# Performance work log

Hardware: AMD Instinct MI355X
Metric: run time of the kernel (lower is better)

The kernel has to match this reference:

```python
import jax, jax.numpy as jnp
import numpy as np

BS, N, FIN = 128, 320, 1
H1, F1 = 8, 18   # layer-1 heads / hidden
H2, F2 = 4, 46   # layer-2 heads / hidden
D1 = H1 * F1     # 144
D2 = H2 * F2     # 184
FC = (104, 45, 84)
ALPHA = 0.2
NEG = -9e15


def _xavier(key, shape):
    fan_in, fan_out = shape[-2], shape[-1]
    s = 1.414 * np.sqrt(2.0 / (fan_in + fan_out))
    return jax.random.normal(key, shape, dtype=jnp.float32) * s


def setup_inputs() -> dict:
    key = jax.random.key(0)
    ks = jax.random.split(key, 20)
    xnodes = jax.random.normal(ks[0], (BS, N, FIN), dtype=jnp.float32)
    adj = (jax.random.uniform(ks[1], (N, N)) < 0.1).astype(jnp.float32)
    adj = jnp.maximum(adj, jnp.eye(N, dtype=jnp.float32))
    inp = {
        'xnodes': xnodes,
        'adj': adj,
        'W1': _xavier(ks[2], (H1, FIN, F1)),
        'a1': _xavier(ks[3], (H1, 2 * F1)),
        'W2': _xavier(ks[4], (H2, D1, F2)),
        'a2': _xavier(ks[5], (H2, 2 * F2)),
        'p1w': _xavier(ks[6], (D1, 1))[:, 0],
        'p1b': jnp.zeros((), jnp.float32),
        'p2w': _xavier(ks[7], (D2, 1))[:, 0],
        'p2b': jnp.zeros((), jnp.float32),
        'e1w': _xavier(ks[8], (3 * N, FC[0])),
        'e1b': jnp.zeros((FC[0],), jnp.float32),
        'e2w': _xavier(ks[9], (FC[0], FC[1])),
        'e2b': jnp.zeros((FC[1],), jnp.float32),
        'e3w': _xavier(ks[10], (FC[1], FC[2])),
        'e3b': jnp.zeros((FC[2],), jnp.float32),
        'cw': _xavier(ks[11], (FC[2], 1))[:, 0],
        'cb': jnp.zeros((), jnp.float32),
    }
    return inp


def _gat(x, adj_mask, W, a):
    """Multi-head GAT layer (all heads vectorized).
    x: [b,n,fin], W: [h,fin,f], a: [h,2f], adj_mask: [n,n] bool.
    Score e_ij = leakyrelu(a_src.h_i + a_dst.h_j) == concat-matmul of the
    original, without materializing the [b,n,n,2f] tensor.
    """
    h = jnp.einsum('bni,hif->bhnf', x, W)              # [b,h,n,f]
    f = h.shape[-1]
    es = jnp.einsum('bhnf,hf->bhn', h, a[:, :f])       # source term
    ed = jnp.einsum('bhnf,hf->bhn', h, a[:, f:])       # dest term
    e = jax.nn.leaky_relu(es[:, :, :, None] + ed[:, :, None, :], ALPHA)
    e = jnp.where(adj_mask[None, None], e, NEG)
    att = jax.nn.softmax(e, axis=-1)                   # [b,h,n,n]
    hp = jnp.einsum('bhnm,bhmf->bhnf', att, h)
    out = jax.nn.elu(hp)                               # concat=True
    b = out.shape[0]
    return out.transpose(0, 2, 1, 3).reshape(b, out.shape[2], -1)  # [b,n,h*f]


def reference(xnodes, adj, W1, a1, W2, a2, p1w, p1b, p2w, p2b,
              e1w, e1b, e2w, e2b, e3w, e3b, cw, cb):
    mask = adj > 0
    x0 = jnp.mean(xnodes, axis=-1)                     # [b,n]
    x = _gat(xnodes, mask, W1, a1)                     # [b,n,144]
    x1 = x @ p1w + p1b                                 # pool1 -> [b,n]
    x = _gat(x, mask, W2, a2)                          # [b,n,184]
    x2 = x @ p2w + p2b                                 # pool2 -> [b,n]
    x_concat = jnp.concatenate([x0, x1, x2], axis=1)   # [b,3n]
    h = jax.nn.elu(x_concat @ e1w + e1b)
    h = jax.nn.elu(h @ e2w + e2b)
    features = jax.nn.elu(h @ e3w + e3b)               # [b,84]
    hazard = (features @ cw + cb).reshape(-1)          # [b]
    return (x_concat, features, hazard)
```

## Files before the change

### kernel.cpp

```cpp
#include <hip/hip_runtime.h>
#include <hip/hip_bf16.h>
#include <math.h>

#define BS 128
#define NN 320
#define H1 8
#define F1 18
#define D1 144
#define H2C 4
#define F2 46
#define FC0 104
#define FC1 45
#define FC2 84
#define LRA 0.2f
#define DEGCAP 96

typedef __attribute__((ext_vector_type(8))) short bf16x8;
typedef __attribute__((ext_vector_type(4))) float f32x4;

__device__ __forceinline__ float wave_max64(float v) {
    #pragma unroll
    for (int off = 32; off > 0; off >>= 1)
        v = fmaxf(v, __shfl_xor(v, off, 64));
    return v;
}
__device__ __forceinline__ float wave_sum64(float v) {
    #pragma unroll
    for (int off = 32; off > 0; off >>= 1)
        v += __shfl_xor(v, off, 64);
    return v;
}
__device__ __forceinline__ short bfb(float x) {
    __hip_bfloat16 b = __float2bfloat16(x);
    return *(short*)&b;
}

__global__ void k_csr(const float* __restrict__ adj,
                      unsigned short* __restrict__ cols16,
                      unsigned short* __restrict__ colsT16,
                      int* __restrict__ len, int* __restrict__ llo,
                      const float* __restrict__ W1,
                      const float* __restrict__ a1, float* __restrict__ c1s,
                      float* __restrict__ c1d, const float* __restrict__ W2,
                      __hip_bfloat16* __restrict__ Bb) {
    int row = blockIdx.x;
    int lane = threadIdx.x;
    if (row < NN) {
        int base = 0, lo = 0;
        for (int c0 = 0; c0 < NN; c0 += 64) {
            int j = c0 + lane;
            bool p = (j < NN) && (adj[row * NN + j] > 0.f);
            unsigned long long m = __ballot(p);
            if (p) {
                int pos = base + __popcll(m & ((1ull << lane) - 1ull));
                if (pos < DEGCAP) {
                    cols16[row * DEGCAP + pos] = (unsigned short)j;
                    colsT16[pos * NN + row] = (unsigned short)j;
                }
            }
            base += __popcll(m);
            unsigned long long mlo = __ballot(p && j < 160);
            lo += __popcll(mlo);
        }
        if (base > DEGCAP) base = DEGCAP;
        if (lo > DEGCAP) lo = DEGCAP;
        for (int q = base + lane; q < DEGCAP; q += 64) {
            cols16[row * DEGCAP + q] = 0;
            colsT16[q * NN + row] = 0;
        }
        if (lane == 0) { len[row] = base; llo[row] = lo; }
    } else if (row == NN) {
        int h = lane;
        if (h < H1) {
            float s = 0.f, d = 0.f;
            for (int f = 0; f < F1; ++f) {
                float w = W1[h * F1 + f];
                s += w * a1[h * 2 * F1 + f];
                d += w * a1[h * 2 * F1 + F1 + f];
            }
            c1s[h] = s;
            c1d[h] = d;
        }
    } else {
        int idx = (row - NN - 1) * 64 + lane;
        int e = idx & 7;
        int t = idx >> 3;
        int n = t % 192, k8 = t / 192;
        int k = k8 * 8 + e, hh = n / 48, f = n - hh * 48;
        float v = (k < 144 && f < 46) ? W2[(hh * 144 + k) * 46 + f] : 0.f;
        Bb[idx] = __float2bfloat16(v);
    }
}

__global__ __launch_bounds__(320) void k_gat1(
    const float* __restrict__ xn, const unsigned short* __restrict__ colsT16,
    const int* __restrict__ len, const float* __restrict__ W1,
    const float* __restrict__ c1s, const float* __restrict__ c1d,
    const float* __restrict__ p1w, __hip_bfloat16* __restrict__ out1b,
    float* __restrict__ part1) {
    int b = blockIdx.x >> 3, h = blockIdx.x & 7;
    __shared__ float xb[NN], stab[NN];
    __shared__ float w1h[F1], pwl[F1];
    __shared__ float redmax[5], redmin[5];
    int tid = threadIdx.x;
    int wv = tid >> 6, lane = tid & 63;
    float xi = xn[b * NN + tid];
    xb[tid] = xi;
    if (tid < F1) { w1h[tid] = W1[h * F1 + tid]; pwl[tid] = p1w[h * F1 + tid]; }
    int Li = len[tid];
    float mx = wave_max64(xi);
    float mn = -wave_max64(-xi);
    int Lmax = (int)wave_max64((float)Li);
    if (lane == 0) { redmax[wv] = mx; redmin[wv] = mn; }
    __syncthreads();
    float MX = redmax[0], MN = redmin[0];
    #pragma unroll
    for (int q = 1; q < 5; ++q) {
        MX = fmaxf(MX, redmax[q]);
        MN = fminf(MN, redmin[q]);
    }
    float cs = c1s[h], cd = c1d[h];
    float u = xi * cs;
    float mt = u + (cd > 0.f ? cd * MX : cd * MN);
    float m = fmaxf(mt, LRA * mt);
    float num = 0.f, den = 0.f;
    const unsigned short* ct = colsT16 + tid;
    int colv = ct[0];
    for (int j = 0; j < Lmax; ++j) {
        int coln = (j + 1 < Lmax) ? ct[(j + 1) * NN] : 0;
        float xj = xb[colv];
        bool act = j < Li;
        float t = fmaf(xj, cd, u);
        t = fmaxf(t, LRA * t);
        float w = __expf(t - m);
        w = act ? w : 0.f;
        num = fmaf(w, xj, num);
        den += w;
        colv = coln;
    }
    stab[tid] = num / den;
    __syncthreads();
    for (int idx = tid; idx < NN * F1; idx += 320) {
        int row = idx / F1, c = idx - row * F1;
        float v = stab[row] * w1h[c];
        v = v > 0.f ? v : expm1f(v);
        out1b[(size_t)(b * NN + row) * 160 + h * F1 + c] = __float2bfloat16(v);
    }
    if (h == 0) {
        for (int idx = tid; idx < NN * 16; idx += 320) {
            int row = idx >> 4, c = idx & 15;
            out1b[(size_t)(b * NN + row) * 160 + 144 + c] = __float2bfloat16(0.f);
        }
    }
    float part = 0.f;
    float s = stab[tid];
    #pragma unroll
    for (int f = 0; f < F1; ++f) {
        float v = s * w1h[f];
        v = v > 0.f ? v : expm1f(v);
        part = fmaf(v, pwl[f], part);
    }
    part1[(size_t)(b * 8 + h) * NN + tid] = part;
}

__global__ __launch_bounds__(256) void k_gemm2(
    const __hip_bfloat16* __restrict__ A,
    const __hip_bfloat16* __restrict__ Bb,
    const float* __restrict__ a2,
    __hip_bfloat16* __restrict__ h2T,
    float* __restrict__ esp, float* __restrict__ edp) {
    __shared__ __align__(16) __hip_bfloat16 As[64 * 168];
    __shared__ __align__(16) __hip_bfloat16 Bs[20 * 96 * 8];
    __shared__ float a2e[4][48], a2d[4][48];
    int tid = threadIdx.x;
    int mblk = blockIdx.x >> 1, hblk = blockIdx.x & 1;
    int r0 = mblk * 64;
    const uint4* Ag = (const uint4*)(A + (size_t)r0 * 160);
    for (int q = tid; q < 1280; q += 256) {
        int row = q / 20, k8 = q % 20;
        *(uint4*)(As + row * 168 + k8 * 8) = Ag[q];
    }
    const uint4* Bg = (const uint4*)Bb;
    for (int q = tid; q < 1920; q += 256) {
        int k8 = q / 96, nl = q % 96;
        *(uint4*)(Bs + (k8 * 96 + nl) * 8) = Bg[k8 * 192 + hblk * 96 + nl];
    }
    if (tid < 192) {
        int hh = tid / 48, f = tid - hh * 48;
        a2e[hh][f] = f < 46 ? a2[hh * 92 + f] : 0.f;
        a2d[hh][f] = f < 46 ? a2[hh * 92 + 46 + f] : 0.f;
    }
    __syncthreads();
    int wv = tid >> 6, l = tid & 63;
    int lr = l & 15, lq = l >> 4;
    bf16x8 af[5];
    const __hip_bfloat16* arow = As + (wv * 16 + lr) * 168 + lq * 8;
    #pragma unroll
    for (int kc = 0; kc < 5; ++kc)
        af[kc] = *(const bf16x8*)(arow + kc * 32);
    f32x4 acc[6];
    #pragma unroll
    for (int t = 0; t < 6; ++t) acc[t] = (f32x4){0.f, 0.f, 0.f, 0.f};
    #pragma unroll
    for (int t = 0; t < 6; ++t) {
        const __hip_bfloat16* bcol = Bs + (t * 16 + lr) * 8;
        #pragma unroll
        for (int kc = 0; kc < 5; ++kc) {
            bf16x8 bf = *(const bf16x8*)(bcol + (kc * 4 + lq) * 768);
            acc[t] = __builtin_amdgcn_mfma_f32_16x16x32_bf16(af[kc], bf, acc[t], 0, 0, 0);
        }
    }
    int b = r0 / NN;
    int nbase = (r0 % NN) + wv * 16 + lq * 4;
    #pragma unroll
    for (int t = 0; t < 6; ++t) {
        int hh = 2 * hblk + (t >= 3);
        int f = (t % 3) * 16 + lr;
        short4 s4;
        s4.x = bfb(acc[t][0]); s4.y = bfb(acc[t][1]);
        s4.z = bfb(acc[t][2]); s4.w = bfb(acc[t][3]);
        *(short4*)(h2T + ((size_t)(b * 4 + hh) * 48 + f) * NN + nbase) = s4;
    }
    float esa[2][4], eda[2][4];
    #pragma unroll
    for (int hs = 0; hs < 2; ++hs)
        #pragma unroll
        for (int j = 0; j < 4; ++j) { esa[hs][j] = 0.f; eda[hs][j] = 0.f; }
    #pragma unroll
    for (int t = 0; t < 6; ++t) {
        int hs = (t >= 3);
        int hh = 2 * hblk + hs;
        int f = (t % 3) * 16 + lr;
        float ae = a2e[hh][f], ad = a2d[hh][f];
        #pragma unroll
        for (int j = 0; j < 4; ++j) {
            esa[hs][j] = fmaf(acc[t][j], ae, esa[hs][j]);
            eda[hs][j] = fmaf(acc[t][j], ad, eda[hs][j]);
        }
    }
    #pragma unroll
    for (int hs = 0; hs < 2; ++hs)
        #pragma unroll
        for (int j = 0; j < 4; ++j) {
            #pragma unroll
            for (int off = 1; off < 16; off <<= 1) {
                esa[hs][j] += __shfl_xor(esa[hs][j], off, 64);
                eda[hs][j] += __shfl_xor(eda[hs][j], off, 64);
            }
        }
    if (lr == 0) {
        #pragma unroll
        for (int hs = 0; hs < 2; ++hs) {
            int bh = b * 4 + 2 * hblk + hs;
            #pragma unroll
            for (int j = 0; j < 4; ++j) {
                esp[(size_t)hblk * 512 * NN + (size_t)bh * NN + nbase + j] = esa[hs][j];
                edp[(size_t)hblk * 512 * NN + (size_t)bh * NN + nbase + j] = eda[hs][j];
            }
        }
    }
}

__global__ __launch_bounds__(256) void k_gat2(
    const __hip_bfloat16* __restrict__ h2T,
    const float* __restrict__ esp, const float* __restrict__ edp,
    const unsigned short* __restrict__ cols16, const int* __restrict__ len,
    const int* __restrict__ llo,
    const float* __restrict__ p2w, float* __restrict__ part2) {
    int bx = blockIdx.x;
    int bh = bx & 511, tile = bx >> 9;
    int h = bh & 3;
    int r0 = tile * 64;
    __shared__ __align__(16) __hip_bfloat16 P[64][168];
    __shared__ __align__(16) __hip_bfloat16 Hs[48][168];
    __shared__ __align__(16) unsigned short colsL[64][DEGCAP];
    __shared__ float esl[64], denl[64], edl[NN];
    __shared__ float pwl[48];
    __shared__ int s0l[64], s1l[64];
    __shared__ float Mred[4];
    int tid = threadIdx.x, wv = tid >> 6, lane = tid & 63;
    float edmax = -1e30f;
    for (int j = tid; j < NN; j += 256) {
        float ed = edp[(size_t)bh * NN + j] +
                   edp[(size_t)512 * NN + (size_t)bh * NN + j];
        edl[j] = ed;
        edmax = fmaxf(edmax, ed);
    }
    if (tid < 64) {
        esl[tid] = esp[(size_t)bh * NN + r0 + tid] +
                   esp[(size_t)512 * NN + (size_t)bh * NN + r0 + tid];
        s0l[tid] = llo[r0 + tid];
        s1l[tid] = len[r0 + tid];
    }
    if (tid < 48) pwl[tid] = tid < 46 ? p2w[h * F2 + tid] : 0.f;
    const uint4* cg = (const uint4*)(cols16 + (size_t)r0 * DEGCAP);
    for (int q = tid; q < 768; q += 256) ((uint4*)&colsL[0][0])[q] = cg[q];
    float wm = wave_max64(edmax);
    if (lane == 0) Mred[wv] = wm;
    __syncthreads();
    float M = fmaxf(fmaxf(Mred[0], Mred[1]), fmaxf(Mred[2], Mred[3]));
    int lr = lane & 15, lq = lane >> 4;
    int r = lane & 15, e = lane >> 4;
    int row = wv * 16 + r;
    float es = esl[row];
    float t0 = es + M;
    float m = fmaxf(t0, LRA * t0);
    f32x4 acc[3];
    #pragma unroll
    for (int t = 0; t < 3; ++t) acc[t] = (f32x4){0.f, 0.f, 0.f, 0.f};
    for (int p = 0; p < 2; ++p) {
        if (p) __syncthreads();
        for (int q = tid; q < 1344; q += 256)
            ((uint4*)&P[0][0])[q] = (uint4){0u, 0u, 0u, 0u};
        for (int q = tid; q < 960; q += 256) {
            int f = q / 20, c = q - f * 20;
            *(uint4*)(&Hs[f][c * 8]) =
                *(const uint4*)(h2T + ((size_t)bh * 48 + f) * NN + p * 160 + c * 8);
        }
        __syncthreads();
        int s0 = p ? s0l[row] : 0;
        int s1 = p ? s1l[row] : s0l[row];
        int pofs = p * 160;
        float dp = 0.f;
        for (int j = s0 + e; j < s1; j += 4) {
            int col = colsL[row][j];
            float t = es + edl[col];
            t = fmaxf(t, LRA * t);
            float w = __expf(t - m);
            dp += w;
            P[row][col - pofs] = __float2bfloat16(w);
        }
        dp += __shfl_xor(dp, 16, 64);
        dp += __shfl_xor(dp, 32, 64);
        if (e == 0) { if (p) denl[row] += dp; else denl[row] = dp; }
        const __hip_bfloat16* Arow = &P[wv * 16 + lr][lq * 8];
        #pragma unroll
        for (int k = 0; k < 5; ++k) {
            bf16x8 a = *(const bf16x8*)(Arow + k * 32);
            #pragma unroll
            for (int t = 0; t < 3; ++t) {
                bf16x8 bf = *(const bf16x8*)(&Hs[t * 16 + lr][k * 32 + lq * 8]);
                acc[t] = __builtin_amdgcn_mfma_f32_16x16x32_bf16(a, bf, acc[t], 0, 0, 0);
            }
        }
    }
    float inv[4], part[4];
    #pragma unroll
    for (int j = 0; j < 4; ++j) {
        inv[j] = 1.f / denl[wv * 16 + lq * 4 + j];
        part[j] = 0.f;
    }
    #pragma unroll
    for (int t = 0; t < 3; ++t) {
        float pw = pwl[t * 16 + lr];
        #pragma unroll
        for (int j = 0; j < 4; ++j) {
            float v = acc[t][j] * inv[j];
            v = v > 0.f ? v : expm1f(v);
            part[j] = fmaf(v, pw, part[j]);
        }
    }
    #pragma unroll
    for (int j = 0; j < 4; ++j) {
        #pragma unroll
        for (int off = 1; off < 16; off <<= 1)
            part[j] += __shfl_xor(part[j], off, 64);
    }
    if (lr == 0) {
        #pragma unroll
        for (int j = 0; j < 4; ++j)
            part2[(size_t)bh * NN + r0 + wv * 16 + lq * 4 + j] = part[j];
    }
}

__global__ __launch_bounds__(256) void k_head(
    const float* __restrict__ xn, const float* __restrict__ part1,
    const float* __restrict__ part2, const float* __restrict__ p1b,
    const float* __restrict__ p2b, const float* __restrict__ e1w,
    const float* __restrict__ e1b, const float* __restrict__ e2w,
    const float* __restrict__ e2b, const float* __restrict__ e3w,
    const float* __restrict__ e3b, const float* __restrict__ cw,
    const float* __restrict__ cb, float* __restrict__ dout) {
    int b = blockIdx.x;
    int tid = threadIdx.x;
    __shared__ float xc[960];
    __shared__ float e1part[2][FC0];
    __shared__ float h1[FC0];
    __shared__ float hh[FC1];
    __shared__ float ft[FC2];
    for (int t = tid; t < NN; t += 256) {
        float x0 = xn[b * NN + t];
        xc[t] = x0;
        dout[b * 960 + t] = x0;
        float s1 = p1b[0];
        #pragma unroll
        for (int h = 0; h < 8; ++h) s1 += part1[(size_t)(b * 8 + h) * NN + t];
        xc[320 + t] = s1;
        dout[b * 960 + 320 + t] = s1;
        float s2 = p2b[0];
        #pragma unroll
        for (int h = 0; h < 4; ++h) s2 += part2[(size_t)(b * 4 + h) * NN + t];
        xc[640 + t] = s2;
        dout[b * 960 + 640 + t] = s2;
    }
    __syncthreads();
    {
        int half = tid >> 7, o = tid & 127;
        if (o < FC0) {
            float a = 0.f;
            int k0 = half * 480;
            for (int k = k0; k < k0 + 480; ++k)
                a = fmaf(xc[k], e1w[k * FC0 + o], a);
            e1part[half][o] = a;
        }
    }
    __syncthreads();
    if (tid < FC0) {
        float a = e1b[tid] + e1part[0][tid] + e1part[1][tid];
        h1[tid] = a > 0.f ? a : expm1f(a);
    }
    __syncthreads();
    if (tid < FC1) {
        float a = e2b[tid];
        for (int k = 0; k < FC0; ++k) a += h1[k] * e2w[k * FC1 + tid];
        hh[tid] = a > 0.f ? a : expm1f(a);
    }
    __syncthreads();
    if (tid < FC2) {
        float a = e3b[tid];
        for (int k = 0; k < FC1; ++k) a += hh[k] * e3w[k * FC2 + tid];
        a = a > 0.f ? a : expm1f(a);
        ft[tid] = a;
        dout[BS * 960 + b * FC2 + tid] = a;
    }
    __syncthreads();
    if (tid < 64) {
        float v = 0.f;
        for (int t = tid; t < FC2; t += 64) v += ft[t] * cw[t];
        v = wave_sum64(v);
        if (tid == 0) dout[BS * 960 + BS * FC2 + b] = v + cb[0];
    }
}

extern "C" void kernel_launch(void* const* d_in, const int* in_sizes, int n_in,
                              void* d_out, int out_size, void* d_ws,
                              size_t ws_size, hipStream_t stream) {
    const float* xn  = (const float*)d_in[0];
    const float* adj = (const float*)d_in[1];
    const float* W1  = (const float*)d_in[2];
    const float* a1  = (const float*)d_in[3];
    const float* W2  = (const float*)d_in[4];
    const float* a2  = (const float*)d_in[5];
    const float* p1w = (const float*)d_in[6];
    const float* p1b = (const float*)d_in[7];
    const float* p2w = (const float*)d_in[8];
    const float* p2b = (const float*)d_in[9];
    const float* e1w = (const float*)d_in[10];
    const float* e1b = (const float*)d_in[11];
    const float* e2w = (const float*)d_in[12];
    const float* e2b = (const float*)d_in[13];
    const float* e3w = (const float*)d_in[14];
    const float* e3b = (const float*)d_in[15];
    const float* cw  = (const float*)d_in[16];
    const float* cb  = (const float*)d_in[17];

    char* ws = (char*)d_ws;
    int*   csr_len  = (int*)ws;
    int*   csr_llo  = (int*)(ws + 1280);
    float* c1s      = (float*)(ws + 2560);
    float* c1d      = (float*)(ws + 2592);
    unsigned short* cols16  = (unsigned short*)(ws + 2688);
    unsigned short* colsT16 = (unsigned short*)(ws + 64128);
    __hip_bfloat16* Bb    = (__hip_bfloat16*)(ws + 125568);
    __hip_bfloat16* out1b = (__hip_bfloat16*)(ws + 187008);
    __hip_bfloat16* h2T   = (__hip_bfloat16*)(ws + 13294208);
    float* esp      = (float*)(ws + 29022848);
    float* edp      = (float*)(ws + 30333568);
    float* part1    = (float*)(ws + 31644288);
    float* part2    = (float*)(ws + 32955008);
    float* dout     = (float*)d_out;

    k_csr<<<NN + 1 + 480, 64, 0, stream>>>(adj, cols16, colsT16, csr_len,
                                           csr_llo, W1, a1, c1s, c1d, W2, Bb);
    k_gat1<<<BS * H1, 320, 0, stream>>>(xn, colsT16, csr_len, W1, c1s, c1d,
                                        p1w, out1b, part1);
    k_gemm2<<<(BS * NN / 64) * 2, 256, 0, stream>>>(out1b, Bb, a2, h2T, esp, edp);
    k_gat2<<<5 * 512, 256, 0, stream>>>(h2T, esp, edp, cols16, csr_len,
                                        csr_llo, p2w, part2);
    k_head<<<BS, 256, 0, stream>>>(xn, part1, part2, p1b, p2b, e1w, e1b,
                                   e2w, e2b, e3w, e3b, cw, cb, dout);
}
```

Measured before the change: 188.6 us.

## Fuse layer-2 projection and attention into one per-(batch,head) kernel, recompute layer-1 output

Layer 1 now stores only the scalar attention aggregate per (batch, head, node) instead of the full bf16 layer-1 activation matrix. A new fused layer-2 kernel recomputes the ELU(s*W1) activations on the fly, runs the W2 projection with MFMA into LDS, computes source/destination scores locally, and then does the sparse-softmax aggregation from LDS in four column bands. This removes the large intermediate global tensors (out1b, h2T, esp/edp) and one kernel launch. In exchange the grid shrinks to 512 blocks with a big LDS footprint, which may limit occupancy, and the expm1 work is recomputed for every layer-2 head.

```diff
diff --git a/kernel.cpp b/kernel.cpp
--- a/kernel.cpp
+++ b/kernel.cpp
@@ -6,7 +6,6 @@
 #define NN 320
 #define H1 8
 #define F1 18
-#define D1 144
 #define H2C 4
 #define F2 46
 #define FC0 104
@@ -14,6 +13,7 @@
 #define FC2 84
 #define LRA 0.2f
 #define DEGCAP 96
+#define PW 104
 
 typedef __attribute__((ext_vector_type(8))) short bf16x8;
 typedef __attribute__((ext_vector_type(4))) float f32x4;
@@ -24,12 +24,6 @@
         v = fmaxf(v, __shfl_xor(v, off, 64));
     return v;
 }
-__device__ __forceinline__ float wave_sum64(float v) {
-    #pragma unroll
-    for (int off = 32; off > 0; off >>= 1)
-        v += __shfl_xor(v, off, 64);
-    return v;
-}
 __device__ __forceinline__ short bfb(float x) {
     __hip_bfloat16 b = __float2bfloat16(x);
     return *(short*)&b;
@@ -38,15 +32,14 @@
 __global__ void k_csr(const float* __restrict__ adj,
                       unsigned short* __restrict__ cols16,
                       unsigned short* __restrict__ colsT16,
-                      int* __restrict__ len, int* __restrict__ llo,
-                      const float* __restrict__ W1,
+                      int4* __restrict__ meta, const float* __restrict__ W1,
                       const float* __restrict__ a1, float* __restrict__ c1s,
                       float* __restrict__ c1d, const float* __restrict__ W2,
                       __hip_bfloat16* __restrict__ Bb) {
     int row = blockIdx.x;
     int lane = threadIdx.x;
     if (row < NN) {
-        int base = 0, lo = 0;
+        int base = 0, c96 = 0, c192 = 0, c288 = 0;
         for (int c0 = 0; c0 < NN; c0 += 64) {
             int j = c0 + lane;
             bool p = (j < NN) && (adj[row * NN + j] > 0.f);
@@ -59,16 +52,19 @@
                 }
             }
             base += __popcll(m);
-            unsigned long long mlo = __ballot(p && j < 160);
-            lo += __popcll(mlo);
+            c96  += __popcll(__ballot(p && j < 96));
+            c192 += __popcll(__ballot(p && j < 192));
+            c288 += __popcll(__ballot(p && j < 288));
         }
         if (base > DEGCAP) base = DEGCAP;
-        if (lo > DEGCAP) lo = DEGCAP;
+        if (c96 > DEGCAP) c96 = DEGCAP;
+        if (c192 > DEGCAP) c192 = DEGCAP;
+        if (c288 > DEGCAP) c288 = DEGCAP;
         for (int q = base + lane; q < DEGCAP; q += 64) {
             cols16[row * DEGCAP + q] = 0;
             colsT16[q * NN + row] = 0;
         }
-        if (lane == 0) { len[row] = base; llo[row] = lo; }
+        if (lane == 0) meta[row] = make_int4(c96, c192, c288, base);
     } else if (row == NN) {
         int h = lane;
         if (h < H1) {
@@ -92,14 +88,14 @@
     }
 }
 
-__global__ __launch_bounds__(320) void k_gat1(
+__global__ __launch_bounds__(320) void k_l1(
     const float* __restrict__ xn, const unsigned short* __restrict__ colsT16,
-    const int* __restrict__ len, const float* __restrict__ W1,
+    const int4* __restrict__ meta, const float* __restrict__ W1,
     const float* __restrict__ c1s, const float* __restrict__ c1d,
-    const float* __restrict__ p1w, __hip_bfloat16* __restrict__ out1b,
+    const float* __restrict__ p1w, float* __restrict__ sg,
     float* __restrict__ part1) {
     int b = blockIdx.x >> 3, h = blockIdx.x & 7;
-    __shared__ float xb[NN], stab[NN];
+    __shared__ float xb[NN];
     __shared__ float w1h[F1], pwl[F1];
     __shared__ float redmax[5], redmin[5];
     int tid = threadIdx.x;
@@ -107,7 +103,7 @@
     float xi = xn[b * NN + tid];
     xb[tid] = xi;
     if (tid < F1) { w1h[tid] = W1[h * F1 + tid]; pwl[tid] = p1w[h * F1 + tid]; }
-    int Li = len[tid];
+    int Li = meta[tid].w;
     float mx = wave_max64(xi);
     float mn = -wave_max64(-xi);
     int Lmax = (int)wave_max64((float)Li);
@@ -138,22 +134,9 @@
         den += w;
         colv = coln;
     }
-    stab[tid] = num / den;
-    __syncthreads();
-    for (int idx = tid; idx < NN * F1; idx += 320) {
-        int row = idx / F1, c = idx - row * F1;
-        float v = stab[row] * w1h[c];
-        v = v > 0.f ? v : expm1f(v);
-        out1b[(size_t)(b * NN + row) * 160 + h * F1 + c] = __float2bfloat16(v);
-    }
-    if (h == 0) {
-        for (int idx = tid; idx < NN * 16; idx += 320) {
-            int row = idx >> 4, c = idx & 15;
-            out1b[(size_t)(b * NN + row) * 160 + 144 + c] = __float2bfloat16(0.f);
-        }
-    }
+    float s = num / den;
+    sg[(size_t)(b * 8 + h) * NN + tid] = s;
     float part = 0.f;
-    float s = stab[tid];
     #pragma unroll
     for (int f = 0; f < F1; ++f) {
         float v = s * w1h[f];
@@ -163,213 +146,199 @@
     part1[(size_t)(b * 8 + h) * NN + tid] = part;
 }
 
-__global__ __launch_bounds__(256) void k_gemm2(
-    const __hip_bfloat16* __restrict__ A,
-    const __hip_bfloat16* __restrict__ Bb,
-    const float* __restrict__ a2,
-    __hip_bfloat16* __restrict__ h2T,
-    float* __restrict__ esp, float* __restrict__ edp) {
-    __shared__ __align__(16) __hip_bfloat16 As[64 * 168];
-    __shared__ __align__(16) __hip_bfloat16 Bs[20 * 96 * 8];
-    __shared__ float a2e[4][48], a2d[4][48];
-    int tid = threadIdx.x;
-    int mblk = blockIdx.x >> 1, hblk = blockIdx.x & 1;
-    int r0 = mblk * 64;
-    const uint4* Ag = (const uint4*)(A + (size_t)r0 * 160);
-    for (int q = tid; q < 1280; q += 256) {
-        int row = q / 20, k8 = q % 20;
-        *(uint4*)(As + row * 168 + k8 * 8) = Ag[q];
-    }
-    const uint4* Bg = (const uint4*)Bb;
-    for (int q = tid; q < 1920; q += 256) {
-        int k8 = q / 96, nl = q % 96;
-        *(uint4*)(Bs + (k8 * 96 + nl) * 8) = Bg[k8 * 192 + hblk * 96 + nl];
-    }
-    if (tid < 192) {
-        int hh = tid / 48, f = tid - hh * 48;
-        a2e[hh][f] = f < 46 ? a2[hh * 92 + f] : 0.f;
-        a2d[hh][f] = f < 46 ? a2[hh * 92 + 46 + f] : 0.f;
-    }
-    __syncthreads();
-    int wv = tid >> 6, l = tid & 63;
-    int lr = l & 15, lq = l >> 4;
-    bf16x8 af[5];
-    const __hip_bfloat16* arow = As + (wv * 16 + lr) * 168 + lq * 8;
+__global__ __launch_bounds__(256) void k_l2(
+    const float* __restrict__ sg, const unsigned short* __restrict__ cols16,
+    const int4* __restrict__ meta, const __hip_bfloat16* __restrict__ Bb,
+    const float* __restrict__ W1, const float* __restrict__ a2,
+    const float* __restrict__ p2w, float* __restrict__ part2) {
+    int bh = blockIdx.x;
+    int b = bh >> 2, h = bh & 3;
+    __shared__ __align__(16) __hip_bfloat16 HT[48][328];
+    __shared__ __align__(16) __hip_bfloat16 AsP[4][16][PW];
+    __shared__ __align__(16) unsigned short colsW[4][16][DEGCAP];
+    __shared__ float sglW[4][8][16];
+    __shared__ float esl[NN], edl[NN];
+    __shared__ float denW[4][16];
+    __shared__ float w1l[8][F1];
+    __shared__ float pwl[48], a2e[48], a2d[48];
+    __shared__ float Mred[4];
+    int tid = threadIdx.x, wv = tid >> 6, lane = tid & 63;
+    int lr = lane & 15, lq = lane >> 4;
+    if (tid < 48) {
+        pwl[tid] = tid < 46 ? p2w[h * F2 + tid] : 0.f;
+        a2e[tid] = tid < 46 ? a2[h * 92 + tid] : 0.f;
+        a2d[tid] = tid < 46 ? a2[h * 92 + 46 + tid] : 0.f;
+    }
+    if (tid < 144) {
+        int hh = tid / F1, f = tid - hh * F1;
+        w1l[hh][f] = W1[hh * F1 + f];
+    }
+    bf16x8 bq[5][3];
     #pragma unroll
     for (int kc = 0; kc < 5; ++kc)
-        af[kc] = *(const bf16x8*)(arow + kc * 32);
-    f32x4 acc[6];
-    #pragma unroll
-    for (int t = 0; t < 6; ++t) acc[t] = (f32x4){0.f, 0.f, 0.f, 0.f};
-    #pragma unroll
-    for (int t = 0; t < 6; ++t) {
-        const __hip_bfloat16* bcol = Bs + (t * 16 + lr) * 8;
-        #pragma unroll
-        for (int kc = 0; kc < 5; ++kc) {
-            bf16x8 bf = *(const bf16x8*)(bcol + (kc * 4 + lq) * 768);
-            acc[t] = __builtin_amdgcn_mfma_f32_16x16x32_bf16(af[kc], bf, acc[t], 0, 0, 0);
-        }
-    }
-    int b = r0 / NN;
-    int nbase = (r0 % NN) + wv * 16 + lq * 4;
-    #pragma unroll
-    for (int t = 0; t < 6; ++t) {
-        int hh = 2 * hblk + (t >= 3);
-        int f = (t % 3) * 16 + lr;
-        short4 s4;
-        s4.x = bfb(acc[t][0]); s4.y = bfb(acc[t][1]);
-        s4.z = bfb(acc[t][2]); s4.w = bfb(acc[t][3]);
-        *(short4*)(h2T + ((size_t)(b * 4 + hh) * 48 + f) * NN + nbase) = s4;
-    }
-    float esa[2][4], eda[2][4];
-    #pragma unroll
-    for (int hs = 0; hs < 2; ++hs)
-        #pragma unroll
-        for (int j = 0; j < 4; ++j) { esa[hs][j] = 0.f; eda[hs][j] = 0.f; }
-    #pragma unroll
-    for (int t = 0; t < 6; ++t) {
-        int hs = (t >= 3);
-        int hh = 2 * hblk + hs;
-        int f = (t % 3) * 16 + lr;
-        float ae = a2e[hh][f], ad = a2d[hh][f];
+        #pragma unroll
+        for (int t = 0; t < 3; ++t)
+            bq[kc][t] = *(const bf16x8*)(Bb +
+                (size_t)(((kc * 4 + lq) * 192) + h * 48 + t * 16 + lr) * 8);
+    __syncthreads();
+    for (int tile = 0; tile < 5; ++tile) {
+        int r0 = tile * 64;
+        for (int q = lane; q < 128; q += 64) {
+            int hh = q >> 4, row = q & 15;
+            sglW[wv][hh][row] = sg[(size_t)(b * 8 + hh) * NN + r0 + wv * 16 + row];
+        }
+        f32x4 acc[3];
+        #pragma unroll
+        for (int t = 0; t < 3; ++t) acc[t] = (f32x4){0.f, 0.f, 0.f, 0.f};
+        #pragma unroll
+        for (int sp = 0; sp < 2; ++sp) {
+            const int nch = sp ? 2 : 3;
+            #pragma unroll
+            for (int j = 0; j < nch; ++j) {
+                int chunk = (sp ? 12 : 0) + lq + 4 * j;
+                int cb = chunk * 8;
+                bf16x8 pv;
+                #pragma unroll
+                for (int e = 0; e < 8; ++e) {
+                    unsigned c = cb + e;
+                    float v = 0.f;
+                    if (c < 144) {
+                        unsigned hh = c / 18, f = c - hh * 18;
+                        v = sglW[wv][hh][lr] * w1l[hh][f];
+                        v = v > 0.f ? v : expm1f(v);
+                    }
+                    pv[e] = bfb(v);
+                }
+                *(bf16x8*)&AsP[wv][lr][cb - sp * 96] = pv;
+            }
+            const int nkc = sp ? 2 : 3;
+            #pragma unroll
+            for (int kc2 = 0; kc2 < nkc; ++kc2) {
+                bf16x8 a = *(const bf16x8*)&AsP[wv][lr][kc2 * 32 + lq * 8];
+                int gkc = sp ? 3 + kc2 : kc2;
+                #pragma unroll
+                for (int t = 0; t < 3; ++t)
+                    acc[t] = __builtin_amdgcn_mfma_f32_16x16x32_bf16(
+                        a, bq[gkc][t], acc[t], 0, 0, 0);
+            }
+        }
+        int node = r0 + wv * 16 + lq * 4;
+        #pragma unroll
+        for (int t = 0; t < 3; ++t) {
+            short4 s4;
+            s4.x = bfb(acc[t][0]); s4.y = bfb(acc[t][1]);
+            s4.z = bfb(acc[t][2]); s4.w = bfb(acc[t][3]);
+            *(short4*)&HT[t * 16 + lr][node] = s4;
+        }
+        float esa[4] = {0.f, 0.f, 0.f, 0.f}, eda[4] = {0.f, 0.f, 0.f, 0.f};
+        #pragma unroll
+        for (int t = 0; t < 3; ++t) {
+            float ae = a2e[t * 16 + lr], ad = a2d[t * 16 + lr];
+            #pragma unroll
+            for (int j = 0; j < 4; ++j) {
+                esa[j] = fmaf(acc[t][j], ae, esa[j]);
+                eda[j] = fmaf(acc[t][j], ad, eda[j]);
+            }
+        }
         #pragma unroll
         for (int j = 0; j < 4; ++j) {
-            esa[hs][j] = fmaf(acc[t][j], ae, esa[hs][j]);
-            eda[hs][j] = fmaf(acc[t][j], ad, eda[hs][j]);
-        }
-    }
-    #pragma unroll
-    for (int hs = 0; hs < 2; ++hs)
-        #pragma unroll
-        for (int j = 0; j < 4; ++j) {
             #pragma unroll
             for (int off = 1; off < 16; off <<= 1) {
-                esa[hs][j] += __shfl_xor(esa[hs][j], off, 64);
-                eda[hs][j] += __shfl_xor(eda[hs][j], off, 64);
-            }
-        }
-    if (lr == 0) {
-        #pragma unroll
-        for (int hs = 0; hs < 2; ++hs) {
-            int bh = b * 4 + 2 * hblk + hs;
+                esa[j] += __shfl_xor(esa[j], off, 64);
+                eda[j] += __shfl_xor(eda[j], off, 64);
+            }
+        }
+        if (lr == 0) {
             #pragma unroll
             for (int j = 0; j < 4; ++j) {
-                esp[(size_t)hblk * 512 * NN + (size_t)bh * NN + nbase + j] = esa[hs][j];
-                edp[(size_t)hblk * 512 * NN + (size_t)bh * NN + nbase + j] = eda[hs][j];
-            }
-        }
-    }
-}
-
-__global__ __launch_bounds__(256) void k_gat2(
-    const __hip_bfloat16* __restrict__ h2T,
-    const float* __restrict__ esp, const float* __restrict__ edp,
-    const unsigned short* __restrict__ cols16, const int* __restrict__ len,
-    const int* __restrict__ llo,
-    const float* __restrict__ p2w, float* __restrict__ part2) {
-    int bx = blockIdx.x;
-    int bh = bx & 511, tile = bx >> 9;
-    int h = bh & 3;
-    int r0 = tile * 64;
-    __shared__ __align__(16) __hip_bfloat16 P[64][168];
-    __shared__ __align__(16) __hip_bfloat16 Hs[48][168];
-    __shared__ __align__(16) unsigned short colsL[64][DEGCAP];
-    __shared__ float esl[64], denl[64], edl[NN];
-    __shared__ float pwl[48];
-    __shared__ int s0l[64], s1l[64];
-    __shared__ float Mred[4];
-    int tid = threadIdx.x, wv = tid >> 6, lane = tid & 63;
+                esl[node + j] = esa[j];
+                edl[node + j] = eda[j];
+            }
+        }
+    }
+    __syncthreads();
     float edmax = -1e30f;
-    for (int j = tid; j < NN; j += 256) {
-        float ed = edp[(size_t)bh * NN + j] +
-                   edp[(size_t)512 * NN + (size_t)bh * NN + j];
-        edl[j] = ed;
-        edmax = fmaxf(edmax, ed);
-    }
-    if (tid < 64) {
-        esl[tid] = esp[(size_t)bh * NN + r0 + tid] +
-                   esp[(size_t)512 * NN + (size_t)bh * NN + r0 + tid];
-        s0l[tid] = llo[r0 + tid];
-        s1l[tid] = len[r0 + tid];
-    }
-    if (tid < 48) pwl[tid] = tid < 46 ? p2w[h * F2 + tid] : 0.f;
-    const uint4* cg = (const uint4*)(cols16 + (size_t)r0 * DEGCAP);
-    for (int q = tid; q < 768; q += 256) ((uint4*)&colsL[0][0])[q] = cg[q];
+    for (int i = tid; i < NN; i += 256) edmax = fmaxf(edmax, edl[i]);
     float wm = wave_max64(edmax);
     if (lane == 0) Mred[wv] = wm;
     __syncthreads();
     float M = fmaxf(fmaxf(Mred[0], Mred[1]), fmaxf(Mred[2], Mred[3]));
-    int lr = lane & 15, lq = lane >> 4;
-    int r = lane & 15, e = lane >> 4;
-    int row = wv * 16 + r;
-    float es = esl[row];
-    float t0 = es + M;
-    float m = fmaxf(t0, LRA * t0);
-    f32x4 acc[3];
-    #pragma unroll
-    for (int t = 0; t < 3; ++t) acc[t] = (f32x4){0.f, 0.f, 0.f, 0.f};
-    for (int p = 0; p < 2; ++p) {
-        if (p) __syncthreads();
-        for (int q = tid; q < 1344; q += 256)
-            ((uint4*)&P[0][0])[q] = (uint4){0u, 0u, 0u, 0u};
-        for (int q = tid; q < 960; q += 256) {
-            int f = q / 20, c = q - f * 20;
-            *(uint4*)(&Hs[f][c * 8]) =
-                *(const uint4*)(h2T + ((size_t)bh * 48 + f) * NN + p * 160 + c * 8);
-        }
-        __syncthreads();
-        int s0 = p ? s0l[row] : 0;
-        int s1 = p ? s1l[row] : s0l[row];
-        int pofs = p * 160;
+    for (int tile = 0; tile < 5; ++tile) {
+        int r0 = tile * 64;
+        for (int q = lane; q < 192; q += 64) {
+            int rr = q / 12, c8 = q - rr * 12;
+            *(uint4*)&colsW[wv][rr][c8 * 8] =
+                *(const uint4*)(cols16 + (size_t)(r0 + wv * 16 + rr) * DEGCAP + c8 * 8);
+        }
+        int i = r0 + wv * 16 + lr;
+        int4 mt = meta[i];
+        int sb0 = mt.x, sb1 = mt.y, sb2 = mt.z, sb3 = mt.w;
+        float es = esl[i];
+        float t0 = es + M;
+        float m = fmaxf(t0, LRA * t0);
+        f32x4 acc[3];
+        #pragma unroll
+        for (int t = 0; t < 3; ++t) acc[t] = (f32x4){0.f, 0.f, 0.f, 0.f};
         float dp = 0.f;
-        for (int j = s0 + e; j < s1; j += 4) {
-            int col = colsL[row][j];
-            float t = es + edl[col];
-            t = fmaxf(t, LRA * t);
-            float w = __expf(t - m);
-            dp += w;
-            P[row][col - pofs] = __float2bfloat16(w);
+        #pragma unroll
+        for (int pass = 0; pass < 4; ++pass) {
+            for (int q = lane; q < 208; q += 64) {
+                int rr = q / 13, cc = q - rr * 13;
+                *(uint4*)&AsP[wv][rr][cc * 8] = (uint4){0u, 0u, 0u, 0u};
+            }
+            int s0 = pass == 0 ? 0 : (pass == 1 ? sb0 : (pass == 2 ? sb1 : sb2));
+            int s1 = pass == 0 ? sb0 : (pass == 1 ? sb1 : (pass == 2 ? sb2 : sb3));
+            int pofs = pass * 96;
+            for (int j = s0 + lq; j < s1; j += 4) {
+                int col = colsW[wv][lr][j];
+                float t = es + edl[col];
+                t = fmaxf(t, LRA * t);
+                float w = __expf(t - m);
+                dp += w;
+                AsP[wv][lr][col - pofs] = __float2bfloat16(w);
+            }
+            const int nkf = (pass < 3) ? 3 : 1;
+            #pragma unroll
+            for (int kf = 0; kf < nkf; ++kf) {
+                bf16x8 a = *(const bf16x8*)&AsP[wv][lr][kf * 32 + lq * 8];
+                #pragma unroll
+                for (int t = 0; t < 3; ++t) {
+                    bf16x8 bb = *(const bf16x8*)&HT[t * 16 + lr][pofs + kf * 32 + lq * 8];
+                    acc[t] = __builtin_amdgcn_mfma_f32_16x16x32_bf16(
+                        a, bb, acc[t], 0, 0, 0);
+                }
+            }
         }
         dp += __shfl_xor(dp, 16, 64);
         dp += __shfl_xor(dp, 32, 64);
-        if (e == 0) { if (p) denl[row] += dp; else denl[row] = dp; }
-        const __hip_bfloat16* Arow = &P[wv * 16 + lr][lq * 8];
-        #pragma unroll
-        for (int k = 0; k < 5; ++k) {
-            bf16x8 a = *(const bf16x8*)(Arow + k * 32);
-            #pragma unroll
-            for (int t = 0; t < 3; ++t) {
-                bf16x8 bf = *(const bf16x8*)(&Hs[t * 16 + lr][k * 32 + lq * 8]);
-                acc[t] = __builtin_amdgcn_mfma_f32_16x16x32_bf16(a, bf, acc[t], 0, 0, 0);
-            }
-        }
-    }
-    float inv[4], part[4];
-    #pragma unroll
-    for (int j = 0; j < 4; ++j) {
-        inv[j] = 1.f / denl[wv * 16 + lq * 4 + j];
-        part[j] = 0.f;
-    }
-    #pragma unroll
-    for (int t = 0; t < 3; ++t) {
-        float pw = pwl[t * 16 + lr];
+        if (lq == 0) denW[wv][lr] = dp;
+        float inv[4], part[4];
         #pragma unroll
         for (int j = 0; j < 4; ++j) {
-            float v = acc[t][j] * inv[j];
-            v = v > 0.f ? v : expm1f(v);
-            part[j] = fmaf(v, pw, part[j]);
-        }
-    }
-    #pragma unroll
-    for (int j = 0; j < 4; ++j) {
-        #pragma unroll
-        for (int off = 1; off < 16; off <<= 1)
-            part[j] += __shfl_xor(part[j], off, 64);
-    }
-    if (lr == 0) {
-        #pragma unroll
-        for (int j = 0; j < 4; ++j)
-            part2[(size_t)bh * NN + r0 + wv * 16 + lq * 4 + j] = part[j];
+            inv[j] = 1.f / denW[wv][lq * 4 + j];
+            part[j] = 0.f;
+        }
+        #pragma unroll
+        for (int t = 0; t < 3; ++t) {
+            float pw = pwl[t * 16 + lr];
+            #pragma unroll
+            for (int j = 0; j < 4; ++j) {
+                float v = acc[t][j] * inv[j];
+                v = v > 0.f ? v : expm1f(v);
+                part[j] = fmaf(v, pw, part[j]);
+            }
+        }
+        #pragma unroll
+        for (int j = 0; j < 4; ++j) {
+            #pragma unroll
+            for (int off = 1; off < 16; off <<= 1)
+                part[j] += __shfl_xor(part[j], off, 64);
+        }
+        if (lr == 0) {
+            #pragma unroll
+            for (int j = 0; j < 4; ++j)
+                part2[(size_t)bh * NN + r0 + wv * 16 + lq * 4 + j] = part[j];
+        }
     }
 }
 
@@ -437,7 +406,8 @@
     if (tid < 64) {
         float v = 0.f;
         for (int t = tid; t < FC2; t += 64) v += ft[t] * cw[t];
-        v = wave_sum64(v);
+        #pragma unroll
+        for (int off = 32; off > 0; off >>= 1) v += __shfl_xor(v, off, 64);
         if (tid == 0) dout[BS * 960 + BS * FC2 + b] = v + cb[0];
     }
 }
@@ -465,28 +435,22 @@
     const float* cb  = (const float*)d_in[17];
 
     char* ws = (char*)d_ws;
-    int*   csr_len  = (int*)ws;
-    int*   csr_llo  = (int*)(ws + 1280);
-    float* c1s      = (float*)(ws + 2560);
-    float* c1d      = (float*)(ws + 2592);
-    unsigned short* cols16  = (unsigned short*)(ws + 2688);
-    unsigned short* colsT16 = (unsigned short*)(ws + 64128);
-    __hip_bfloat16* Bb    = (__hip_bfloat16*)(ws + 125568);
-    __hip_bfloat16* out1b = (__hip_bfloat16*)(ws + 187008);
-    __hip_bfloat16* h2T   = (__hip_bfloat16*)(ws + 13294208);
-    float* esp      = (float*)(ws + 29022848);
-    float* edp      = (float*)(ws + 30333568);
-    float* part1    = (float*)(ws + 31644288);
-    float* part2    = (float*)(ws + 32955008);
+    int4*  meta     = (int4*)ws;
+    float* c1s      = (float*)(ws + 5120);
+    float* c1d      = (float*)(ws + 5152);
+    unsigned short* cols16  = (unsigned short*)(ws + 5248);
+    unsigned short* colsT16 = (unsigned short*)(ws + 66688);
+    __hip_bfloat16* Bb = (__hip_bfloat16*)(ws + 128128);
+    float* sg       = (float*)(ws + 189568);
+    float* part1    = (float*)(ws + 1500288);
+    float* part2    = (float*)(ws + 2811008);
     float* dout     = (float*)d_out;
 
-    k_csr<<<NN + 1 + 480, 64, 0, stream>>>(adj, cols16, colsT16, csr_len,
-                                           csr_llo, W1, a1, c1s, c1d, W2, Bb);
-    k_gat1<<<BS * H1, 320, 0, stream>>>(xn, colsT16, csr_len, W1, c1s, c1d,
-                                        p1w, out1b, part1);
-    k_gemm2<<<(BS * NN / 64) * 2, 256, 0, stream>>>(out1b, Bb, a2, h2T, esp, edp);
-    k_gat2<<<5 * 512, 256, 0, stream>>>(h2T, esp, edp, cols16, csr_len,
-                                        csr_llo, p2w, part2);
+    k_csr<<<NN + 1 + 480, 64, 0, stream>>>(adj, cols16, colsT16, meta,
+                                           W1, a1, c1s, c1d, W2, Bb);
+    k_l1<<<BS * H1, 320, 0, stream>>>(xn, colsT16, meta, W1, c1s, c1d,
+                                      p1w, sg, part1);
+    k_l2<<<BS * H2C, 256, 0, stream>>>(sg, cols16, meta, Bb, W1, a2, p2w, part2);
     k_head<<<BS, 256, 0, stream>>>(xn, part1, part2, p1b, p2b, e1w, e1b,
                                    e2w, e2b, e3w, e3b, cw, cb, dout);
 }
```

Result: faster. 181.5 us (-3.7%).
